# Optimization experiments

Hardware: AMD Instinct MI355X
Metric: run time of the kernel (lower is better)

## Reference

```python
import jax, jax.numpy as jnp
import numpy as np

DIM = 1024
DIM_FEAT = 384
HIDDEN = 1024
HEADS = 16
D_HEAD = HIDDEN // HEADS
SCALE = D_HEAD ** -0.5
EPS = 1e-5


def _layernorm(x, g, b):
    mu = jnp.mean(x, axis=-1, keepdims=True)
    var = jnp.var(x, axis=-1, keepdims=True)
    return (x - mu) * jax.lax.rsqrt(var + EPS) * g + b


def _split_heads(t):
    b, n, _ = t.shape
    return t.reshape(b, n, HEADS, D_HEAD).transpose(0, 2, 1, 3)  # b h n d


def _merge_heads(t):
    b, h, n, d = t.shape
    return t.transpose(0, 2, 1, 3).reshape(b, n, h * d)


def _attn(q, k, v):
    dots = jnp.einsum('bhnd,bhmd->bhnm', q, k) * SCALE
    attn = jax.nn.softmax(dots, axis=-1)
    return jnp.einsum('bhnm,bhmd->bhnd', attn, v)


def setup_inputs() -> dict:
    key = jax.random.key(0)
    ks = jax.random.split(key, 10)
    B, N = 2, 2048
    s = lambda fan: 1.0 / np.sqrt(fan)
    return {
        'x': jax.random.normal(ks[0], (B, N, DIM), jnp.float32),
        'feature': jax.random.normal(ks[1], (B, N, DIM_FEAT), jnp.float32),
        'norm_g': jnp.ones((DIM,), jnp.float32),
        'norm_b': jnp.zeros((DIM,), jnp.float32),
        'W_cq': jax.random.normal(ks[2], (DIM, HIDDEN), jnp.float32) * s(DIM),
        'W_ckv': jax.random.normal(ks[3], (DIM_FEAT, 2 * HIDDEN), jnp.float32) * s(DIM_FEAT),
        'W_sqkv': jax.random.normal(ks[4], (DIM, 3 * HIDDEN), jnp.float32) * s(DIM),
        'ffn_g': jnp.ones((DIM,), jnp.float32),
        'ffn_b': jnp.zeros((DIM,), jnp.float32),
        'W1': jax.random.normal(ks[5], (DIM, 4 * DIM), jnp.float32) * s(DIM),
        'b1': jnp.zeros((4 * DIM,), jnp.float32),
        'W2': jax.random.normal(ks[6], (4 * DIM, DIM), jnp.float32) * s(4 * DIM),
        'b2': jnp.zeros((DIM,), jnp.float32),
    }


def reference(x, feature, norm_g, norm_b, W_cq, W_ckv, W_sqkv, ffn_g, ffn_b, W1, b1, W2, b2):
    # cross attention
    xn = _layernorm(x, norm_g, norm_b)
    q = _split_heads(xn @ W_cq)
    kv = feature @ W_ckv
    k, v = jnp.split(kv, 2, axis=-1)
    cross = _merge_heads(_attn(q, _split_heads(k), _split_heads(v))) + x
    # self attention (shared norm)
    cn = _layernorm(cross, norm_g, norm_b)
    qkv = cn @ W_sqkv
    sq, sk, sv = (_split_heads(t) for t in jnp.split(qkv, 3, axis=-1))
    self_tok = _merge_heads(_attn(sq, sk, sv)) + cross
    # FFN with its own layernorm
    h = _layernorm(self_tok, ffn_g, ffn_b)
    h = jax.nn.gelu(h @ W1 + b1, approximate=False)
    out = h @ W2 + b2
    return out + self_tok
```

## Files before the change

kernel.cpp:

```cpp
#include <hip/hip_runtime.h>
#include <math.h>
#include <stdint.h>

typedef __attribute__((ext_vector_type(8)))  short   short8;
typedef __attribute__((ext_vector_type(4)))  short   short4v;
typedef __attribute__((ext_vector_type(8)))  __bf16  bf16x8;
typedef __attribute__((ext_vector_type(4)))  float   f32x4;
typedef __attribute__((ext_vector_type(16))) float   f32x16;

__device__ __forceinline__ unsigned short f2b(float f) {
    union { float f; unsigned u; } v; v.f = f;
    unsigned r = v.u + 0x7FFF + ((v.u >> 16) & 1);
    return (unsigned short)(r >> 16);
}

__device__ __forceinline__ f32x4 mfma_bf16(bf16x8 a, bf16x8 b, f32x4 c) {
    return __builtin_amdgcn_mfma_f32_16x16x32_bf16(a, b, c, 0, 0, 0);
}

__device__ __forceinline__ f32x16 mfma32(bf16x8 a, bf16x8 b, f32x16 c) {
    return __builtin_amdgcn_mfma_f32_32x32x16_bf16(a, b, c, 0, 0, 0);
}

__device__ __forceinline__ unsigned cvt_pk_bf16(float lo, float hi) {
    unsigned r;
    asm volatile("v_cvt_pk_bf16_f32 %0, %1, %2" : "=v"(r) : "v"(lo), "v"(hi));
    return r;
}

__device__ __forceinline__ void gload_lds16(const unsigned short* g, unsigned short* l) {
    __builtin_amdgcn_global_load_lds(
        (const __attribute__((address_space(1))) void*)g,
        (__attribute__((address_space(3))) void*)l,
        16, 0, 0);
}

template <int N>
__device__ __forceinline__ void wait_vmcnt() {
    if constexpr (N == 0)       asm volatile("s_waitcnt vmcnt(0)" ::: "memory");
    else if constexpr (N == 4)  asm volatile("s_waitcnt vmcnt(4)" ::: "memory");
    else if constexpr (N == 6)  asm volatile("s_waitcnt vmcnt(6)" ::: "memory");
    else if constexpr (N == 8)  asm volatile("s_waitcnt vmcnt(8)" ::: "memory");
    else                        static_assert(N == 0 || N == 4 || N == 6 || N == 8, "add vmcnt case");
}

#define QSCALE 0.18033688011112042592f

__global__ __launch_bounds__(256) void wconv_t(const float* __restrict__ W,
                                               unsigned short* __restrict__ Wt,
                                               int K, int N) {
    __shared__ float tile[32][33];
    int bk = blockIdx.x * 32;
    int bn = blockIdx.y * 32;
    int tx = threadIdx.x & 31, ty = threadIdx.x >> 5;
#pragma unroll
    for (int i = 0; i < 4; ++i) {
        int r = ty + i * 8;
        tile[r][tx] = W[(size_t)(bk + r) * N + bn + tx];
    }
    __syncthreads();
#pragma unroll
    for (int i = 0; i < 4; ++i) {
        int r = ty + i * 8;
        Wt[(size_t)(bn + r) * K + bk + tx] = f2b(tile[tx][r]);
    }
}

__global__ __launch_bounds__(256) void fconv(const float* __restrict__ in,
                                             unsigned short* __restrict__ out, int n4) {
    int i = blockIdx.x * 256 + threadIdx.x;
    if (i >= n4) return;
    f32x4 v = ((const f32x4*)in)[i];
    short4v o;
    o.x = (short)f2b(v.x); o.y = (short)f2b(v.y);
    o.z = (short)f2b(v.z); o.w = (short)f2b(v.w);
    ((short4v*)out)[i] = o;
}

__global__ __launch_bounds__(256) void lnorm(const float* __restrict__ x,
                                             const float* __restrict__ g,
                                             const float* __restrict__ bta,
                                             unsigned short* __restrict__ out) {
    int row = blockIdx.x;
    const f32x4* xr = (const f32x4*)(x + (size_t)row * 1024);
    int t = threadIdx.x;
    f32x4 v = xr[t];
    float s  = v.x + v.y + v.z + v.w;
    float s2 = v.x * v.x + v.y * v.y + v.z * v.z + v.w * v.w;
#pragma unroll
    for (int m = 1; m < 64; m <<= 1) {
        s  += __shfl_xor(s, m);
        s2 += __shfl_xor(s2, m);
    }
    __shared__ float rs[8];
    int w = t >> 6;
    if ((t & 63) == 0) { rs[w] = s; rs[4 + w] = s2; }
    __syncthreads();
    s  = rs[0] + rs[1] + rs[2] + rs[3];
    s2 = rs[4] + rs[5] + rs[6] + rs[7];
    float mean = s * (1.0f / 1024.0f);
    float var  = s2 * (1.0f / 1024.0f) - mean * mean;
    float rstd = rsqrtf(var + 1e-5f);
    f32x4 gv = ((const f32x4*)g)[t];
    f32x4 bv = ((const f32x4*)bta)[t];
    short4v o;
    o.x = (short)f2b((v.x - mean) * rstd * gv.x + bv.x);
    o.y = (short)f2b((v.y - mean) * rstd * gv.y + bv.y);
    o.z = (short)f2b((v.z - mean) * rstd * gv.z + bv.z);
    o.w = (short)f2b((v.w - mean) * rstd * gv.w + bv.w);
    ((short4v*)(out + (size_t)row * 1024))[t] = o;
}

template <int WM, int WN, int MI, int NI, int EPI, bool SCQ>
__global__ __launch_bounds__(WM * WN * 64, 2)
void gemm8(const unsigned short* __restrict__ A,
           const unsigned short* __restrict__ Bt,
           void* __restrict__ C,
           const float* __restrict__ bias,
           const float* __restrict__ resid,
           int M, int N, int K, int scale_cols) {
    constexpr int BM = WM * MI * 16;
    constexpr int BN = WN * NI * 16;
    constexpr int THREADS = WM * WN * 64;
    constexpr int ROWS = THREADS / 8;
    constexpr int IA = BM / ROWS;
    constexpr int IB = BN / ROWS;

    const int nwg = gridDim.x;
    const int nby = N / BN;
    int flat = blockIdx.x;
    int wk = (flat & 7) * (nwg >> 3) + (flat >> 3);
    const int m0 = (wk / nby) * BM;
    const int n0 = (wk % nby) * BN;

    __shared__ unsigned short As[2][BM * 64];
    __shared__ unsigned short Bs[2][BN * 64];

    const int tid  = threadIdx.x;
    const int lane = tid & 63;
    const int wid  = tid >> 6;
    const int wm = wid / WN, wn = wid % WN;
    const int l15 = lane & 15, q4 = lane >> 4, xw = lane & 7;

    const int sr = tid >> 3;
    const int sg = (tid & 7) ^ (sr & 7);

    const unsigned short* ag = A  + (size_t)(m0 + sr) * K + sg * 8;
    const unsigned short* bg = Bt + (size_t)(n0 + sr) * K + sg * 8;

    f32x4 acc[MI][NI] = {};

    auto STAGE = [&](int d, int t) {
        const int k0 = t * 64;
#pragma unroll
        for (int i = 0; i < IA; ++i)
            gload_lds16(ag + (size_t)(i * ROWS) * K + k0, &As[d][i * ROWS * 64 + tid * 8]);
#pragma unroll
        for (int i = 0; i < IB; ++i)
            gload_lds16(bg + (size_t)(i * ROWS) * K + k0, &Bs[d][i * ROWS * 64 + tid * 8]);
    };

    const int NT = K >> 6;
    STAGE(0, 0);

    for (int t = 0; t < NT; ++t) {
        const int c = t & 1;
        if (t + 1 < NT) STAGE(c ^ 1, t + 1);
        __builtin_amdgcn_sched_barrier(0);
        if (t + 1 < NT) wait_vmcnt<IA + IB>();
        else            wait_vmcnt<0>();
        __builtin_amdgcn_s_barrier();
        __builtin_amdgcn_sched_barrier(0);
#pragma unroll
        for (int h = 0; h < 2; ++h) {
            bf16x8 a[MI], b[NI];
            const int gsl = h * 4 + q4;
#pragma unroll
            for (int mi = 0; mi < MI; ++mi)
                a[mi] = *(const bf16x8*)&As[c][(wm * MI * 16 + mi * 16 + l15) * 64 + ((gsl ^ xw) << 3)];
#pragma unroll
            for (int ni = 0; ni < NI; ++ni)
                b[ni] = *(const bf16x8*)&Bs[c][(wn * NI * 16 + ni * 16 + l15) * 64 + ((gsl ^ xw) << 3)];
            __builtin_amdgcn_s_setprio(1);
#pragma unroll
            for (int mi = 0; mi < MI; ++mi)
#pragma unroll
                for (int ni = 0; ni < NI; ++ni)
                    acc[mi][ni] = mfma_bf16(a[mi], b[ni], acc[mi][ni]);
            __builtin_amdgcn_s_setprio(0);
        }
        __builtin_amdgcn_sched_barrier(0);
        __builtin_amdgcn_s_barrier();
    }

    const int rb = m0 + wm * MI * 16 + q4 * 4;
    const int cb = n0 + wn * NI * 16 + l15;
    float bv[NI];
    if (EPI >= 1) {
#pragma unroll
        for (int ni = 0; ni < NI; ++ni) bv[ni] = bias[cb + ni * 16];
    }
#pragma unroll
    for (int mi = 0; mi < MI; ++mi) {
#pragma unroll
        for (int r = 0; r < 4; ++r) {
            const int row = rb + mi * 16 + r;
#pragma unroll
            for (int ni = 0; ni < NI; ++ni) {
                const int col = cb + ni * 16;
                float v = acc[mi][ni][r];
                if (EPI == 0) {
                    if (SCQ && col < scale_cols) v *= QSCALE;
                    ((unsigned short*)C)[(size_t)row * N + col] = f2b(v);
                } else if (EPI == 1) {
                    v += bv[ni];
                    v = 0.5f * v * (1.0f + erff(v * 0.70710678118f));
                    ((unsigned short*)C)[(size_t)row * N + col] = f2b(v);
                } else {
                    v += bv[ni] + resid[(size_t)row * N + col];
                    ((float*)C)[(size_t)row * N + col] = v;
                }
            }
        }
    }
}

__global__ __launch_bounds__(256) void vtrans(const unsigned short* __restrict__ src,
                                              unsigned short* __restrict__ dst,
                                              int src_stride, int col_off) {
    int n0 = blockIdx.x * 64;
    int bh = blockIdx.y;
    int b = bh >> 4, h = bh & 15;
    __shared__ unsigned short t[64][65];
    int tx = threadIdx.x & 63, ty = threadIdx.x >> 6;
    const unsigned short* s = src + (size_t)(b * 2048 + n0) * src_stride + col_off + h * 64;
#pragma unroll
    for (int i = 0; i < 16; ++i) {
        int n = ty * 16 + i;
        t[n][tx] = s[(size_t)n * src_stride + tx];
    }
    __syncthreads();
    unsigned short* d = dst + (size_t)bh * 64 * 2048 + n0;
#pragma unroll
    for (int i = 0; i < 16; ++i) {
        int dd = ty * 16 + i;
        d[(size_t)dd * 2048 + tx] = t[tx][dd];
    }
}

__global__ __launch_bounds__(256) void attn(const unsigned short* __restrict__ Q, int q_stride, int q_off,
                                            const unsigned short* __restrict__ Kp, int k_stride, int k_off,
                                            const unsigned short* __restrict__ Vt,
                                            const float* __restrict__ res,
                                            float* __restrict__ out) {
    const int bid = blockIdx.x;
    const int slot = bid >> 3;
    const int bh = (bid & 7) * 4 + (slot >> 4);
    const int qt = slot & 15;
    const int b = bh >> 4, h = bh & 15;
    const int lane = threadIdx.x & 63, w = threadIdx.x >> 6;
    const int l31 = lane & 31, l5 = lane >> 5;

    __shared__ unsigned short Ks[3][64 * 64];
    __shared__ unsigned short Vs[3][64 * 64];

    const int q0 = qt * 128 + w * 32;

    const unsigned short* qp = Q + (size_t)(b * 2048 + q0 + l31) * q_stride + q_off + h * 64 + l5 * 8;
    bf16x8 qf[4];
#pragma unroll
    for (int i = 0; i < 4; ++i) qf[i] = *(const bf16x8*)&qp[i * 16];

    const unsigned short* kg = Kp + (size_t)(b * 2048) * k_stride + k_off + h * 64;
    const unsigned short* vg = Vt + (size_t)bh * 64 * 2048;

    const int sgrow = lane >> 3;
    const int sgcol = (((lane & 7) ^ sgrow) << 3);

    f32x16 oacc[2] = {};
    float m = -1e30f, l = 0.f;

    const int kxor = (l31 & 7) << 3;

    auto STAGE = [&](int d, int t) {
        const int n0s = t * 64;
#pragma unroll
        for (int t8 = 0; t8 < 2; ++t8) {
            const int rb = w * 16 + t8 * 8;
            gload_lds16(kg + (size_t)(n0s + rb + sgrow) * k_stride + sgcol, &Ks[d][rb * 64]);
            gload_lds16(vg + (size_t)(rb + sgrow) * 2048 + n0s + sgcol,     &Vs[d][rb * 64]);
        }
    };

    STAGE(0, 0);
    STAGE(1, 1);

    for (int t = 0; t < 32; ++t) {
        const int cur = t % 3;
        if (t + 2 < 32) STAGE((t + 2) % 3, t + 2);
        __builtin_amdgcn_sched_barrier(0);
        if (t + 2 < 32)      wait_vmcnt<8>();
        else if (t + 1 < 32) wait_vmcnt<4>();
        else                 wait_vmcnt<0>();
        __builtin_amdgcn_s_barrier();
        __builtin_amdgcn_sched_barrier(0);

        const unsigned short* Kc = &Ks[cur][0];
        const unsigned short* Vc = &Vs[cur][0];

        bf16x8 kf[2][4];
#pragma unroll
        for (int ks = 0; ks < 2; ++ks)
#pragma unroll
            for (int i = 0; i < 4; ++i)
                kf[ks][i] = *(const bf16x8*)&Kc[(ks * 32 + l31) * 64 + ((i * 16 + l5 * 8) ^ kxor)];

        f32x16 s0 = {}, s1 = {};
        __builtin_amdgcn_s_setprio(1);
#pragma unroll
        for (int i = 0; i < 4; ++i) s0 = mfma32(kf[0][i], qf[i], s0);
#pragma unroll
        for (int i = 0; i < 4; ++i) s1 = mfma32(kf[1][i], qf[i], s1);
        __builtin_amdgcn_s_setprio(0);

        bf16x8 vf[2][4];
#pragma unroll
        for (int dh = 0; dh < 2; ++dh)
#pragma unroll
            for (int c = 0; c < 4; ++c)
                vf[dh][c] = *(const bf16x8*)&Vc[(dh * 32 + l31) * 64 + ((c * 16 + l5 * 8) ^ kxor)];

        float tr[16];
#pragma unroll
        for (int r = 0; r < 16; ++r) tr[r] = fmaxf(s0[r], s1[r]);
#pragma unroll
        for (int off = 8; off >= 1; off >>= 1)
#pragma unroll
            for (int r = 0; r < off; ++r) tr[r] = fmaxf(tr[r], tr[r + off]);
        float mx = fmaxf(tr[0], __shfl_xor(tr[0], 32));
        if (!__all(mx - m <= 8.f)) {
            float mnew = fmaxf(m, mx);
            float al = __builtin_amdgcn_exp2f(m - mnew);
            m = mnew;
            l *= al;
#pragma unroll
            for (int dh = 0; dh < 2; ++dh)
#pragma unroll
                for (int r = 0; r < 16; ++r) oacc[dh][r] *= al;
        }
        float p0[16], p1[16];
#pragma unroll
        for (int r = 0; r < 16; ++r) p0[r] = __builtin_amdgcn_exp2f(s0[r] - m);
#pragma unroll
        for (int r = 0; r < 16; ++r) p1[r] = __builtin_amdgcn_exp2f(s1[r] - m);
        float sm[16];
#pragma unroll
        for (int r = 0; r < 16; ++r) sm[r] = p0[r] + p1[r];
#pragma unroll
        for (int off = 8; off >= 1; off >>= 1)
#pragma unroll
            for (int r = 0; r < off; ++r) sm[r] += sm[r + off];
        l += sm[0] + __shfl_xor(sm[0], 32);

        bf16x8 pf[4];
#pragma unroll
        for (int half = 0; half < 2; ++half) {
            const float* p = half ? p1 : p0;
#pragma unroll
            for (int c = 0; c < 2; ++c) {
                unsigned a0 = cvt_pk_bf16(p[8 * c + 0], p[8 * c + 1]);
                unsigned a1 = cvt_pk_bf16(p[8 * c + 4], p[8 * c + 5]);
                unsigned b0 = cvt_pk_bf16(p[8 * c + 2], p[8 * c + 3]);
                unsigned b1 = cvt_pk_bf16(p[8 * c + 6], p[8 * c + 7]);
                asm volatile("v_permlane32_swap_b32 %0, %1" : "+v"(a0), "+v"(a1));
                asm volatile("v_permlane32_swap_b32 %0, %1" : "+v"(b0), "+v"(b1));
                union { unsigned u[4]; bf16x8 v; } pu;
                pu.u[0] = a0; pu.u[1] = b0; pu.u[2] = a1; pu.u[3] = b1;
                pf[half * 2 + c] = pu.v;
            }
        }

        __builtin_amdgcn_s_setprio(1);
#pragma unroll
        for (int dh = 0; dh < 2; ++dh)
#pragma unroll
            for (int c = 0; c < 4; ++c)
                oacc[dh] = mfma32(vf[dh][c], pf[c], oacc[dh]);
        __builtin_amdgcn_s_setprio(0);

        __builtin_amdgcn_s_barrier();
    }

    const float inv = 1.0f / l;
    const size_t rowoff = (size_t)(b * 2048 + q0 + l31) * 1024 + h * 64;
#pragma unroll
    for (int dh = 0; dh < 2; ++dh) {
#pragma unroll
        for (int g = 0; g < 4; ++g) {
            const int col = dh * 32 + g * 8 + l5 * 4;
            f32x4 rv = *(const f32x4*)&res[rowoff + col];
            f32x4 ov;
#pragma unroll
            for (int r = 0; r < 4; ++r) ov[r] = oacc[dh][g * 4 + r] * inv + rv[r];
            *(f32x4*)&out[rowoff + col] = ov;
        }
    }
}

extern "C" void kernel_launch(void* const* d_in, const int* in_sizes, int n_in,
                              void* d_out, int out_size, void* d_ws, size_t ws_size,
                              hipStream_t stream) {
    const float* x      = (const float*)d_in[0];
    const float* feat   = (const float*)d_in[1];
    const float* norm_g = (const float*)d_in[2];
    const float* norm_b = (const float*)d_in[3];
    const float* W_cq   = (const float*)d_in[4];
    const float* W_ckv  = (const float*)d_in[5];
    const float* W_sqkv = (const float*)d_in[6];
    const float* ffn_g  = (const float*)d_in[7];
    const float* ffn_b  = (const float*)d_in[8];
    const float* W1     = (const float*)d_in[9];
    const float* b1     = (const float*)d_in[10];
    const float* W2     = (const float*)d_in[11];
    const float* b2     = (const float*)d_in[12];
    float* out = (float*)d_out;

    char* ws = (char*)d_ws;
    unsigned short* wq_t   = (unsigned short*)(ws + (size_t)(0u)   * (1u << 20));
    unsigned short* wkv_t  = (unsigned short*)(ws + (size_t)(2u)   * (1u << 20));
    unsigned short* wqkv_t = (unsigned short*)(ws + (size_t)(4u)   * (1u << 20));
    unsigned short* w1_t   = (unsigned short*)(ws + (size_t)(10u)  * (1u << 20));
    unsigned short* w2_t   = (unsigned short*)(ws + (size_t)(18u)  * (1u << 20));
    unsigned short* featb  = (unsigned short*)(ws + (size_t)(26u)  * (1u << 20));
    unsigned short* t0     = (unsigned short*)(ws + (size_t)(29u)  * (1u << 20));
    float*          cross  = (float*)        (ws + (size_t)(37u)  * (1u << 20));
    unsigned short* qb     = (unsigned short*)(ws + (size_t)(53u)  * (1u << 20));
    unsigned short* kvb    = (unsigned short*)(ws + (size_t)(61u)  * (1u << 20));
    unsigned short* qkvb   = (unsigned short*)(ws + (size_t)(77u)  * (1u << 20));
    unsigned short* vtb    = (unsigned short*)(ws + (size_t)(101u) * (1u << 20));
    unsigned short* h1     = (unsigned short*)(ws + (size_t)(53u)  * (1u << 20));

    wconv_t<<<dim3(1024 / 32, 1024 / 32), 256, 0, stream>>>(W_cq,   wq_t,   1024, 1024);
    wconv_t<<<dim3(384 / 32,  2048 / 32), 256, 0, stream>>>(W_ckv,  wkv_t,  384,  2048);
    wconv_t<<<dim3(1024 / 32, 3072 / 32), 256, 0, stream>>>(W_sqkv, wqkv_t, 1024, 3072);
    wconv_t<<<dim3(1024 / 32, 4096 / 32), 256, 0, stream>>>(W1,     w1_t,   1024, 4096);
    wconv_t<<<dim3(4096 / 32, 1024 / 32), 256, 0, stream>>>(W2,     w2_t,   4096, 1024);
    fconv<<<dim3((4096 * 384 / 4) / 256), 256, 0, stream>>>(feat, featb, 4096 * 384 / 4);

    lnorm<<<4096, 256, 0, stream>>>(x, norm_g, norm_b, t0);
    gemm8<2, 2, 4, 2, 0, true ><<<512, 256, 0, stream>>>(t0,    wq_t,  qb,  nullptr, nullptr, 4096, 1024, 1024, 1024);
    gemm8<2, 2, 4, 4, 0, false><<<512, 256, 0, stream>>>(featb, wkv_t, kvb, nullptr, nullptr, 4096, 2048, 384,  0);
    vtrans<<<dim3(32, 32), 256, 0, stream>>>(kvb, vtb, 2048, 1024);
    attn<<<512, 256, 0, stream>>>(qb, 1024, 0, kvb, 2048, 0, vtb, x, cross);

    lnorm<<<4096, 256, 0, stream>>>(cross, norm_g, norm_b, t0);
    gemm8<2, 2, 4, 2, 0, true ><<<1536, 256, 0, stream>>>(t0, wqkv_t, qkvb, nullptr, nullptr, 4096, 3072, 1024, 1024);
    vtrans<<<dim3(32, 32), 256, 0, stream>>>(qkvb, vtb, 3072, 2048);
    attn<<<512, 256, 0, stream>>>(qkvb, 3072, 0, qkvb, 3072, 1024, vtb, cross, out);

    lnorm<<<4096, 256, 0, stream>>>(out, ffn_g, ffn_b, t0);
    gemm8<2, 2, 4, 4, 1, false><<<1024, 256, 0, stream>>>(t0, w1_t, h1, b1, nullptr, 4096, 4096, 1024, 0);
    gemm8<2, 2, 4, 2, 2, false><<<512, 256, 0, stream>>>(h1, w2_t, out, b2, (const float*)out, 4096, 1024, 4096, 0);
}
```

Measured before the change: 354.0 us.

## Add 256x256-tile 512-thread GEMM for QKV and FFN1; double-buffer attention

Introduces a new GEMM kernel with 256x256 output tiles, 8 waves, and double-buffered LDS with prefetch interleaved into the MFMA phases. It is used for the self-attention QKV projection and the first FFN projection. Larger tiles raise operand reuse and cut global traffic per flop, but the grid drops to 192 and 256 blocks, which may underfill the 256 CUs, and the kernel needs 128KB of LDS. Attention K/V staging also shrinks from triple to double buffering, which lowers LDS use but leaves less prefetch slack.

Measured after the change: 348.0 us. Within noise of the previous version (-1.7%).

```diff
diff --git a/kernel.cpp b/kernel.cpp
--- a/kernel.cpp
+++ b/kernel.cpp
@@ -225,6 +225,119 @@
     }
 }
 
+template <int EPI, bool SCQ>
+__global__ __launch_bounds__(512, 2)
+void gemm256(const unsigned short* __restrict__ A,
+             const unsigned short* __restrict__ Bt,
+             void* __restrict__ C,
+             const float* __restrict__ bias,
+             const float* __restrict__ resid,
+             int M, int N, int K, int scale_cols) {
+    const int nby = N / 256;
+    const int nwg = gridDim.x;
+    int flat = blockIdx.x;
+    int wk = (flat & 7) * (nwg >> 3) + (flat >> 3);
+    const int m0 = (wk / nby) * 256;
+    const int n0 = (wk % nby) * 256;
+
+    __shared__ unsigned short As[2][256 * 64];
+    __shared__ unsigned short Bs[2][256 * 64];
+
+    const int tid  = threadIdx.x;
+    const int lane = tid & 63;
+    const int wid  = tid >> 6;
+    const int wm = wid >> 2, wn = wid & 3;
+    const int l15 = lane & 15, q4 = lane >> 4, xw = lane & 7;
+
+    const int sr = tid >> 3;
+    const int sg = (tid & 7) ^ (sr & 7);
+
+    const unsigned short* ag = A  + (size_t)(m0 + sr) * K + sg * 8;
+    const unsigned short* bg = Bt + (size_t)(n0 + sr) * K + sg * 8;
+
+    f32x4 acc[8][4] = {};
+
+#define SA256(d, t, i) gload_lds16(ag + (size_t)((i) * 64) * K + (t) * 64, &As[d][(i) * 4096 + tid * 8])
+#define SB256(d, t, i) gload_lds16(bg + (size_t)((i) * 64) * K + (t) * 64, &Bs[d][(i) * 4096 + tid * 8])
+
+    const int NT = K >> 6;
+#pragma unroll
+    for (int i = 0; i < 4; ++i) { SA256(0, 0, i); SB256(0, 0, i); }
+    wait_vmcnt<0>();
+    __builtin_amdgcn_s_barrier();
+
+    for (int t = 0; t < NT; ++t) {
+        const int c = t & 1;
+        const bool pf = (t + 1 < NT);
+        bf16x8 breg[4];
+#pragma unroll
+        for (int p = 0; p < 4; ++p) {
+            const int h = p >> 1, mh = p & 1;
+            const int col = ((h * 4 + q4) ^ xw) << 3;
+            if ((p & 1) == 0) {
+#pragma unroll
+                for (int ni = 0; ni < 4; ++ni)
+                    breg[ni] = *(const bf16x8*)&Bs[c][(wn * 64 + ni * 16 + l15) * 64 + col];
+            }
+            bf16x8 a[4];
+#pragma unroll
+            for (int mi = 0; mi < 4; ++mi)
+                a[mi] = *(const bf16x8*)&As[c][(wm * 128 + mh * 64 + mi * 16 + l15) * 64 + col];
+            if (pf) {
+                if (p == 0)      { SA256(c ^ 1, t + 1, 0); SB256(c ^ 1, t + 1, 0); SA256(c ^ 1, t + 1, 1); }
+                else if (p == 1) { SB256(c ^ 1, t + 1, 1); SA256(c ^ 1, t + 1, 2); SB256(c ^ 1, t + 1, 2); }
+                else if (p == 2) { SA256(c ^ 1, t + 1, 3); SB256(c ^ 1, t + 1, 3); }
+            }
+            __builtin_amdgcn_sched_barrier(0);
+            asm volatile("s_waitcnt lgkmcnt(0)" ::: "memory");
+            __builtin_amdgcn_sched_barrier(0);
+            __builtin_amdgcn_s_setprio(1);
+#pragma unroll
+            for (int mi = 0; mi < 4; ++mi)
+#pragma unroll
+                for (int ni = 0; ni < 4; ++ni)
+                    acc[mh * 4 + mi][ni] = mfma_bf16(a[mi], breg[ni], acc[mh * 4 + mi][ni]);
+            __builtin_amdgcn_s_setprio(0);
+            __builtin_amdgcn_sched_barrier(0);
+            if (p == 3) wait_vmcnt<0>();
+            __builtin_amdgcn_s_barrier();
+        }
+    }
+#undef SA256
+#undef SB256
+
+    const int rb = m0 + wm * 128 + q4 * 4;
+    const int cb = n0 + wn * 64 + l15;
+    float bv[4];
+    if (EPI >= 1) {
+#pragma unroll
+        for (int ni = 0; ni < 4; ++ni) bv[ni] = bias[cb + ni * 16];
+    }
+#pragma unroll
+    for (int ai = 0; ai < 8; ++ai) {
+#pragma unroll
+        for (int r = 0; r < 4; ++r) {
+            const int row = rb + ai * 16 + r;
+#pragma unroll
+            for (int ni = 0; ni < 4; ++ni) {
+                const int col = cb + ni * 16;
+                float v = acc[ai][ni][r];
+                if (EPI == 0) {
+                    if (SCQ && col < scale_cols) v *= QSCALE;
+                    ((unsigned short*)C)[(size_t)row * N + col] = f2b(v);
+                } else if (EPI == 1) {
+                    v += bv[ni];
+                    v = 0.5f * v * (1.0f + erff(v * 0.70710678118f));
+                    ((unsigned short*)C)[(size_t)row * N + col] = f2b(v);
+                } else {
+                    v += bv[ni] + resid[(size_t)row * N + col];
+                    ((float*)C)[(size_t)row * N + col] = v;
+                }
+            }
+        }
+    }
+}
+
 __global__ __launch_bounds__(256) void vtrans(const unsigned short* __restrict__ src,
                                               unsigned short* __restrict__ dst,
                                               int src_stride, int col_off) {
@@ -261,8 +374,8 @@
     const int lane = threadIdx.x & 63, w = threadIdx.x >> 6;
     const int l31 = lane & 31, l5 = lane >> 5;
 
-    __shared__ unsigned short Ks[3][64 * 64];
-    __shared__ unsigned short Vs[3][64 * 64];
+    __shared__ unsigned short Ks[2][64 * 64];
+    __shared__ unsigned short Vs[2][64 * 64];
 
     const int q0 = qt * 128 + w * 32;
 
@@ -293,15 +406,13 @@
     };
 
     STAGE(0, 0);
-    STAGE(1, 1);
 
     for (int t = 0; t < 32; ++t) {
-        const int cur = t % 3;
-        if (t + 2 < 32) STAGE((t + 2) % 3, t + 2);
+        const int cur = t & 1;
+        if (t + 1 < 32) STAGE(cur ^ 1, t + 1);
         __builtin_amdgcn_sched_barrier(0);
-        if (t + 2 < 32)      wait_vmcnt<8>();
-        else if (t + 1 < 32) wait_vmcnt<4>();
-        else                 wait_vmcnt<0>();
+        if (t + 1 < 32) wait_vmcnt<4>();
+        else            wait_vmcnt<0>();
         __builtin_amdgcn_s_barrier();
         __builtin_amdgcn_sched_barrier(0);
 
@@ -454,11 +565,11 @@
     attn<<<512, 256, 0, stream>>>(qb, 1024, 0, kvb, 2048, 0, vtb, x, cross);
 
     lnorm<<<4096, 256, 0, stream>>>(cross, norm_g, norm_b, t0);
-    gemm8<2, 2, 4, 2, 0, true ><<<1536, 256, 0, stream>>>(t0, wqkv_t, qkvb, nullptr, nullptr, 4096, 3072, 1024, 1024);
+    gemm256<0, true ><<<192, 512, 0, stream>>>(t0, wqkv_t, qkvb, nullptr, nullptr, 4096, 3072, 1024, 1024);
     vtrans<<<dim3(32, 32), 256, 0, stream>>>(qkvb, vtb, 3072, 2048);
     attn<<<512, 256, 0, stream>>>(qkvb, 3072, 0, qkvb, 3072, 1024, vtb, cross, out);
 
     lnorm<<<4096, 256, 0, stream>>>(out, ffn_g, ffn_b, t0);
-    gemm8<2, 2, 4, 4, 1, false><<<1024, 256, 0, stream>>>(t0, w1_t, h1, b1, nullptr, 4096, 4096, 1024, 0);
+    gemm256<1, false><<<256, 512, 0, stream>>>(t0, w1_t, h1, b1, nullptr, 4096, 4096, 1024, 0);
     gemm8<2, 2, 4, 2, 2, false><<<512, 256, 0, stream>>>(h1, w2_t, out, b2, (const float*)out, 4096, 1024, 4096, 0);
 }
```
